# Optimization experiments

Measured on AMD Instinct MI355X. Metric: run time of the kernel, lower is better.

The kernel has to match this reference:

```python
import jax, jax.numpy as jnp
import numpy as np

B, MAX_OBJS, D = 8, 12, 512
NUM_OBJ, NUM_ACT, NUM_TRS = 37, 6, 3
EMBED = 128
NUM_AA = 100
NUM_CLASSES = 300
ACT_THRES = 0.5
K = MAX_OBJS * NUM_ACT            # 72 candidate (object, action) slots
FINAL_DIM = 2 * (D + 2 * EMBED)   # 1536
# All ordered pairs (i, j), i != j, in lexicographic order. itertools.permutations
# over a sorted index subset is exactly the valid-masked subsequence of this list.
_pairs = np.array([(i, j) for i in range(K) for j in range(K) if i != j], dtype=np.int64)
PAIR_I = jnp.asarray(_pairs[:, 0])
PAIR_J = jnp.asarray(_pairs[:, 1])
P = _pairs.shape[0]               # K*(K-1) = 5112 (static max num pairs)


def setup_inputs() -> dict:
    key = jax.random.key(0)
    ks = jax.random.split(key, 12)
    inp = jax.random.normal(ks[0], (B, MAX_OBJS, D), jnp.float32)
    objmask = jnp.ones((B, MAX_OBJS), jnp.float32)
    # -1 marks 'no composite-action target' for that (obj, act) slot
    AAidxs_tgts = jax.random.randint(ks[1], (B, K), -1, NUM_AA)
    TR_tgts = jax.random.uniform(ks[2], (B, K, K, NUM_TRS), jnp.float32)
    obj_act_lookup = jax.random.randint(ks[3], (NUM_OBJ, NUM_ACT), 0, NUM_AA)
    aa_aa_tr_lookup = jax.random.randint(ks[4], (NUM_AA, NUM_AA, NUM_TRS), 0, NUM_CLASSES)
    s = lambda k, shape: (jax.random.normal(k, shape, jnp.float32) * 0.02)
    return {
        'inp': inp, 'objmask': objmask,
        'TR_tgts': TR_tgts,
        'W_obj': s(ks[5], (NUM_OBJ, D)), 'b_obj': jnp.zeros((NUM_OBJ,), jnp.float32),
        'W_act': s(ks[6], (NUM_ACT, D)), 'b_act': jnp.zeros((NUM_ACT,), jnp.float32),
        'W_tr': s(ks[7], (NUM_TRS, FINAL_DIM)), 'b_tr': jnp.zeros((NUM_TRS,), jnp.float32),
        'W_ne': s(ks[8], (NUM_CLASSES, D)), 'b_ne': jnp.zeros((NUM_CLASSES,), jnp.float32),
        'obj_emb': s(ks[9], (NUM_OBJ, EMBED)), 'act_emb': s(ks[10], (NUM_ACT, EMBED)),
        'AAidxs_tgts': AAidxs_tgts,
        'obj_act_lookup': obj_act_lookup,
        'aa_aa_tr_lookup': aa_aa_tr_lookup,
    }


def reference(inp, objmask, TR_tgts, W_obj, b_obj, W_act, b_act, W_tr, b_tr,
              W_ne, b_ne, obj_emb, act_emb, AAidxs_tgts, obj_act_lookup,
              aa_aa_tr_lookup):
    # training branch (is_eval=False); obj_act_lookup only used in eval branch
    exp_objmask = jnp.repeat(objmask, NUM_ACT, axis=1)                # [B,K]
    masked = inp * objmask[:, :, None]
    pooled = masked.sum(axis=1) / objmask.sum(axis=1, keepdims=True)  # [B,D]
    non_exist_out = pooled @ W_ne.T + b_ne                            # [B,C]
    obj_out = inp @ W_obj.T + b_obj                                   # [B,MO,NO]
    act_out = inp @ W_act.T + b_act                                   # [B,MO,NA]

    posb_action_idxs = jnp.tile(jnp.arange(NUM_ACT), (B, MAX_OBJS))   # [B,K]
    pred_obj_idxs = jnp.repeat(jnp.argmax(obj_out, axis=-1), NUM_ACT, axis=1)  # [B,K]
    posb_inputs = jnp.repeat(inp, NUM_ACT, axis=1)                    # [B,K,D]

    pred_act = (jax.nn.sigmoid(act_out.reshape(B, K)) > ACT_THRES).astype(jnp.float32)
    pred_act = pred_act * exp_objmask
    selected = (pred_act == 1.0) & (AAidxs_tgts != -1)                # [B,K]
    aaidx = jnp.where(selected, AAidxs_tgts, -1)

    posb_obj_emb = obj_emb[pred_obj_idxs]                             # [B,K,E]
    posb_act_emb = act_emb[posb_action_idxs]                          # [B,K,E]
    comp = jnp.concatenate([posb_inputs, posb_obj_emb, posb_act_emb], axis=-1)  # [B,K,FINAL/2]

    # pack valid pairs to the front (stable sort preserves lexicographic order,
    # matching itertools.permutations over the sorted selected index set)
    valid = selected[:, PAIR_I] & selected[:, PAIR_J]                 # [B,P]
    order = jnp.argsort(~valid, axis=1, stable=True)                  # [B,P]
    valid_p = jnp.take_along_axis(valid, order, axis=1)
    i_p = jnp.take_along_axis(jnp.broadcast_to(PAIR_I, (B, P)), order, axis=1)
    j_p = jnp.take_along_axis(jnp.broadcast_to(PAIR_J, (B, P)), order, axis=1)
    b_ix = jnp.arange(B)[:, None]

    pair_out = jnp.where(valid_p[..., None],
                         jnp.concatenate([comp[b_ix, i_p], comp[b_ix, j_p]], axis=-1),
                         -1.0)                                        # [B,P,FINAL_DIM]
    pair_logits = pair_out @ W_tr.T + b_tr                            # [B,P,3]

    aai = aaidx[b_ix, i_p]
    aaj = aaidx[b_ix, j_p]
    ca = aa_aa_tr_lookup[jnp.maximum(aai, 0), jnp.maximum(aaj, 0)]    # [B,P,3]
    ca = jnp.where(valid_p[..., None], ca, -1)
    tr_targets = jnp.where(valid_p[..., None], TR_tgts[b_ix, i_p, j_p], -1.0)

    # diag(logit) @ one_hot(ca) then masked max over pairs == segment max per class
    flat_logit = pair_logits.reshape(B, P * NUM_TRS)
    flat_ca = ca.reshape(B, P * NUM_TRS)
    flat_valid = jnp.repeat(valid_p, NUM_TRS, axis=1)
    seg = jnp.where(flat_valid, flat_ca, NUM_CLASSES)                 # dump invalid to extra segment
    seg_max = jax.vmap(lambda l, s: jax.ops.segment_max(l, s, num_segments=NUM_CLASSES + 1))(
        flat_logit, seg)[:, :NUM_CLASSES]                             # [B,C]
    counts = jax.vmap(lambda s: jax.ops.segment_sum(jnp.ones_like(s), s, num_segments=NUM_CLASSES + 1))(
        seg)[:, :NUM_CLASSES]
    exist = counts > 0
    final_outputs = jnp.where(exist, seg_max, non_exist_out)          # [B,C]

    return final_outputs, pair_logits, tr_targets, act_out, obj_out
```

## Files before the change

kernel.cpp:

```cpp
#include <hip/hip_runtime.h>
#include <hip/hip_bf16.h>

#define Bn    8
#define MO    12
#define Dd    512
#define NOBJ  37
#define NACT  6
#define NTRS  3
#define EMB   128
#define NAA   100
#define NCLS  300
#define Kk    72
#define Pp    5112
#define HALF  768
#define FD    1536

#define OUT_FINAL 0
#define OUT_PLOG  (Bn*NCLS)
#define OUT_TTGT  (OUT_PLOG + Bn*Pp*NTRS)
#define OUT_ACT   (OUT_TTGT + Bn*Pp*NTRS)
#define OUT_OBJ   (OUT_ACT + Bn*Kk)

#define WS_POOL 0
#define WS_OBJ  (WS_POOL + Bn*Dd)
#define WS_ACT  (WS_OBJ + Bn*MO*NOBJ)
#define WS_LINP (WS_ACT + Bn*Kk)
#define WS_EO   (WS_LINP + Bn*MO*6)
#define WS_EA   (WS_EO + NOBJ*6)
#define WS_INV  (WS_EA + NACT*6)
#define WS_NE   (WS_INV + 6)
#define WS_SEG  (WS_NE + Bn*NCLS)
#define WS_PRED (WS_SEG + Bn*NCLS)
#define WS_SEL  (WS_PRED + Bn*MO)
#define WS_AAI  (WS_SEL + Bn*Kk)

__device__ __forceinline__ unsigned fmap(float f) {
  unsigned u = __float_as_uint(f);
  return (u & 0x80000000u) ? ~u : (u | 0x80000000u);
}
__device__ __forceinline__ float funmap(unsigned u) {
  return __uint_as_float((u & 0x80000000u) ? (u & 0x7fffffffu) : ~u);
}

__device__ __forceinline__ float wreduce(float v) {
#pragma unroll
  for (int off = 32; off > 0; off >>= 1) v += __shfl_xor(v, off, 64);
  return v;
}

__device__ __forceinline__ float dot512_wave(const float* __restrict__ a,
                                             const float* __restrict__ b, int lane) {
  const float4* a4 = (const float4*)a;
  const float4* b4 = (const float4*)b;
  float4 x0 = a4[lane], y0 = b4[lane];
  float4 x1 = a4[lane + 64], y1 = b4[lane + 64];
  float s0 = fmaf(x0.x, y0.x, fmaf(x0.y, y0.y, fmaf(x0.z, y0.z, x0.w * y0.w)));
  float s1 = fmaf(x1.x, y1.x, fmaf(x1.y, y1.y, fmaf(x1.z, y1.z, x1.w * y1.w)));
  return wreduce(s0 + s1);
}

__device__ __forceinline__ float dot128_wave(const float* __restrict__ a,
                                             const float* __restrict__ b, int lane) {
  const float2* a2 = (const float2*)a;
  const float2* b2 = (const float2*)b;
  float2 x = a2[lane], y = b2[lane];
  return wreduce(fmaf(x.x, y.x, x.y * y.y));
}

#define AW_OBJ  (Bn*MO*NOBJ)
#define AW_ACT  (AW_OBJ + Bn*Kk)
#define AW_LINP (AW_ACT + Bn*MO*6)
#define AW_EO   (AW_LINP + NOBJ*6)
#define AW_EA   (AW_EO + NACT*6)
#define AW_INV  (AW_EA + NTRS)
#define AW_POOL (AW_INV + Bn*8)
#define AW_ZERO (AW_POOL + 38)

__global__ __launch_bounds__(256) void kA(
    const float* __restrict__ inp, const float* __restrict__ objmask,
    const float* __restrict__ W_obj, const float* __restrict__ b_obj,
    const float* __restrict__ W_act, const float* __restrict__ b_act,
    const float* __restrict__ W_tr, const float* __restrict__ b_tr,
    const float* __restrict__ obj_emb, const float* __restrict__ act_emb,
    float* __restrict__ out, float* __restrict__ ws)
{
  int gt = blockIdx.x * 256 + threadIdx.x;
  int w = gt >> 6, lane = gt & 63;
  if (w < AW_OBJ) {
    int b = w / (MO*NOBJ), r = w % (MO*NOBJ), o = r / NOBJ, c = r % NOBJ;
    float v = dot512_wave(W_obj + c*Dd, inp + (b*MO+o)*Dd, lane) + b_obj[c];
    if (!lane) { out[OUT_OBJ + (b*MO+o)*NOBJ + c] = v; ws[WS_OBJ + (b*MO+o)*NOBJ + c] = v; }
  } else if (w < AW_ACT) {
    int r = w - AW_OBJ, b = r / Kk, k = r % Kk, o = k / NACT, a = k % NACT;
    float v = dot512_wave(W_act + a*Dd, inp + (b*MO+o)*Dd, lane) + b_act[a];
    if (!lane) { out[OUT_ACT + b*Kk + k] = v; ws[WS_ACT + b*Kk + k] = v; }
  } else if (w < AW_LINP) {
    int r = w - AW_ACT, b = r / (MO*6), r2 = r % (MO*6), o = r2 / 6, th = r2 % 6;
    int t = th >> 1, h = th & 1;
    float v = dot512_wave(W_tr + t*FD + h*HALF, inp + (b*MO+o)*Dd, lane);
    if (!lane) ws[WS_LINP + (b*MO+o)*6 + th] = v;
  } else if (w < AW_EO) {
    int r = w - AW_LINP, oc = r / 6, th = r % 6, t = th >> 1, h = th & 1;
    float v = dot128_wave(W_tr + t*FD + h*HALF + Dd, obj_emb + oc*EMB, lane);
    if (!lane) ws[WS_EO + oc*6 + th] = v;
  } else if (w < AW_EA) {
    int r = w - AW_EO, a = r / 6, th = r % 6, t = th >> 1, h = th & 1;
    float v = dot128_wave(W_tr + t*FD + h*HALF + Dd + EMB, act_emb + a*EMB, lane);
    if (!lane) ws[WS_EA + a*6 + th] = v;
  } else if (w < AW_INV) {
    int t = w - AW_EA;
    const float4* w4 = (const float4*)(W_tr + t*FD);
    float s = 0.f;
#pragma unroll
    for (int i = 0; i < 6; ++i) { float4 x = w4[lane + 64*i]; s += x.x + x.y + x.z + x.w; }
    s = wreduce(s);
    if (!lane) ws[WS_INV + t] = b_tr[t] - s;
  } else if (w < AW_POOL) {
    int r = w - AW_INV, b = r >> 3, d = (r & 7)*64 + lane;
    float msum = 0.f, acc = 0.f;
#pragma unroll
    for (int o = 0; o < MO; ++o) {
      float m = objmask[b*MO + o];
      msum += m;
      acc = fmaf(inp[(b*MO+o)*Dd + d], m, acc);
    }
    ws[WS_POOL + b*Dd + d] = acc / msum;
  } else if (w < AW_ZERO) {
    int idx = (w - AW_POOL)*64 + lane;
    if (idx < Bn*NCLS) ((unsigned*)ws)[WS_SEG + idx] = 0u;
  }
}

#define BW_NE (Bn*NCLS)

__global__ __launch_bounds__(256) void kB(
    const float* __restrict__ objmask, const int* __restrict__ AA,
    const float* __restrict__ W_ne, const float* __restrict__ b_ne,
    float* __restrict__ ws)
{
  int gt = blockIdx.x * 256 + threadIdx.x;
  int w = gt >> 6, lane = gt & 63;
  if (w < BW_NE) {
    int b = w / NCLS, c = w % NCLS;
    float v = dot512_wave(W_ne + c*Dd, ws + WS_POOL + b*Dd, lane) + b_ne[c];
    if (!lane) ws[WS_NE + b*NCLS + c] = v;
  } else {
    int t2 = gt - BW_NE*64;
    if (t2 < Bn*MO) {
      int b = t2 / MO, o = t2 % MO;
      const float* p = ws + WS_OBJ + (b*MO+o)*NOBJ;
      float best = p[0]; int bi = 0;
      for (int c = 1; c < NOBJ; ++c) { float v = p[c]; if (v > best) { best = v; bi = c; } }
      ((int*)ws)[WS_PRED + b*MO + o] = bi;
    } else if (t2 < Bn*MO + Bn*Kk) {
      int r = t2 - Bn*MO, b = r / Kk, k = r % Kk, o = k / NACT;
      int aa = AA[b*Kk + k];
      int sel = (ws[WS_ACT + b*Kk + k] > 0.f) && (objmask[b*MO+o] == 1.0f) && (aa != -1);
      ((int*)ws)[WS_SEL + b*Kk + k] = sel;
      ((int*)ws)[WS_AAI + b*Kk + k] = sel ? aa : -1;
    }
  }
}

#define NSLICE 20

__global__ __launch_bounds__(256) void kC(
    const float* __restrict__ TRt, const float* __restrict__ b_tr,
    const int* __restrict__ aalut,
    float* __restrict__ out, float* __restrict__ ws)
{
  __shared__ float s_L[Kk*6];
  __shared__ float s_inv[NTRS];
  __shared__ int s_sel[Kk], s_aa[Kk], s_C[Kk], s_T;

  int b = blockIdx.x / NSLICE, slice = blockIdx.x % NSLICE;
  int tid = threadIdx.x;

  if (tid < Kk) {
    s_sel[tid] = ((const int*)ws)[WS_SEL + b*Kk + tid];
    s_aa[tid]  = ((const int*)ws)[WS_AAI + b*Kk + tid];
  } else if (tid < Kk + NTRS) {
    s_inv[tid - Kk] = ws[WS_INV + (tid - Kk)];
  }
  for (int m = tid; m < Kk*6; m += 256) {
    int k = m / 6, th = m % 6, t = th >> 1, h = th & 1;
    int o = k / NACT, a = k % NACT;
    int po = ((const int*)ws)[WS_PRED + b*MO + o];
    float v = ws[WS_LINP + (b*MO+o)*6 + th] + ws[WS_EO + po*6 + th] + ws[WS_EA + a*6 + th];
    if (h == 0) v += b_tr[t];
    s_L[m] = v;
  }
  __syncthreads();
  if (tid == 0) {
    int c = 0;
    for (int k = 0; k < Kk; ++k) { s_C[k] = c; c += s_sel[k]; }
    s_T = c;
  }
  __syncthreads();

  int T = s_T, Vtot = T*(T-1);
  int q = slice*256 + tid;
  if (q < Pp) {
    float* plog = out + OUT_PLOG + (size_t)b*Pp*NTRS;
    float* ttgt = out + OUT_TTGT + (size_t)b*Pp*NTRS;
    int i = q / (Kk-1);
    int jj = q - i*(Kk-1);
    int j = jj + (jj >= i ? 1 : 0);
    int si = s_sel[i], sj = s_sel[j];
    int vb = s_C[i]*(T-1) + (si ? (s_C[j] - (i < j ? 1 : 0)) : 0);
    bool valid = si && sj;
    int pos = valid ? vb : (Vtot + q - vb);
    float l0, l1, l2;
    if (valid) {
      l0 = s_L[i*6+0] + s_L[j*6+1];
      l1 = s_L[i*6+2] + s_L[j*6+3];
      l2 = s_L[i*6+4] + s_L[j*6+5];
    } else { l0 = s_inv[0]; l1 = s_inv[1]; l2 = s_inv[2]; }
    int ob = pos*3;
    plog[ob+0] = l0; plog[ob+1] = l1; plog[ob+2] = l2;
    if (valid) {
      const float* tr = TRt + (((size_t)b*Kk + i)*Kk + j)*NTRS;
      ttgt[ob+0] = tr[0]; ttgt[ob+1] = tr[1]; ttgt[ob+2] = tr[2];
      int base = (s_aa[i]*NAA + s_aa[j])*NTRS;
      unsigned* seg = (unsigned*)ws + WS_SEG + b*NCLS;
      atomicMax(&seg[aalut[base+0]], fmap(l0));
      atomicMax(&seg[aalut[base+1]], fmap(l1));
      atomicMax(&seg[aalut[base+2]], fmap(l2));
    } else {
      ttgt[ob+0] = -1.f; ttgt[ob+1] = -1.f; ttgt[ob+2] = -1.f;
    }
  }
}

__global__ __launch_bounds__(320) void kD(float* __restrict__ out,
                                          const float* __restrict__ ws)
{
  int b = blockIdx.x, c = threadIdx.x;
  if (c < NCLS) {
    unsigned u = ((const unsigned*)ws)[WS_SEG + b*NCLS + c];
    out[OUT_FINAL + b*NCLS + c] = u ? funmap(u) : ws[WS_NE + b*NCLS + c];
  }
}

extern "C" void kernel_launch(void* const* d_in, const int* in_sizes, int n_in,
                              void* d_out, int out_size, void* d_ws, size_t ws_size,
                              hipStream_t stream) {
  (void)in_sizes; (void)n_in; (void)ws_size; (void)out_size;
  const float* inp      = (const float*)d_in[0];
  const float* objmask  = (const float*)d_in[1];
  const float* TRt      = (const float*)d_in[2];
  const float* W_obj    = (const float*)d_in[3];
  const float* b_obj    = (const float*)d_in[4];
  const float* W_act    = (const float*)d_in[5];
  const float* b_act    = (const float*)d_in[6];
  const float* W_tr     = (const float*)d_in[7];
  const float* b_tr     = (const float*)d_in[8];
  const float* W_ne     = (const float*)d_in[9];
  const float* b_ne     = (const float*)d_in[10];
  const float* obj_emb  = (const float*)d_in[11];
  const float* act_emb  = (const float*)d_in[12];
  const int*   AA       = (const int*)d_in[13];
  const int*   aalut    = (const int*)d_in[15];
  float* out = (float*)d_out;
  float* ws  = (float*)d_ws;

  hipLaunchKernelGGL(kA, dim3((AW_ZERO + 3) / 4), dim3(256), 0, stream,
                     inp, objmask, W_obj, b_obj, W_act, b_act, W_tr, b_tr,
                     obj_emb, act_emb, out, ws);
  hipLaunchKernelGGL(kB, dim3((BW_NE + 11 + 3) / 4), dim3(256), 0, stream,
                     objmask, AA, W_ne, b_ne, ws);
  hipLaunchKernelGGL(kC, dim3(Bn * NSLICE), dim3(256), 0, stream,
                     TRt, b_tr, aalut, out, ws);
  hipLaunchKernelGGL(kD, dim3(Bn), dim3(320), 0, stream, out, ws);
}
```

Before: 97.00 us.

## Fuse pooling, classifier heads and selection into one kernel, dropping a launch

Merges the first two kernels into one. Each object row is loaded once per wave and reused across all object-class and action dot products, and argmax and selection are computed in-wave. The masked mean pooling is recomputed inside every non-exist class wave, so no pooled intermediate goes through workspace. This removes one kernel launch and a global round trip. In exchange there is redundant pooling work (300 times per batch) and longer serial per-wave loops for the object head.

```diff
diff --git a/kernel.cpp b/kernel.cpp
--- a/kernel.cpp
+++ b/kernel.cpp
@@ -21,10 +21,7 @@
 #define OUT_ACT   (OUT_TTGT + Bn*Pp*NTRS)
 #define OUT_OBJ   (OUT_ACT + Bn*Kk)
 
-#define WS_POOL 0
-#define WS_OBJ  (WS_POOL + Bn*Dd)
-#define WS_ACT  (WS_OBJ + Bn*MO*NOBJ)
-#define WS_LINP (WS_ACT + Bn*Kk)
+#define WS_LINP 0
 #define WS_EO   (WS_LINP + Bn*MO*6)
 #define WS_EA   (WS_EO + NOBJ*6)
 #define WS_INV  (WS_EA + NACT*6)
@@ -48,15 +45,19 @@
   return v;
 }
 
+__device__ __forceinline__ float dotW(const float* __restrict__ wrow,
+                                      float4 x0, float4 x1, int lane) {
+  const float4* w4 = (const float4*)wrow;
+  float4 w0 = w4[lane], w1 = w4[lane + 64];
+  float s0 = fmaf(w0.x, x0.x, fmaf(w0.y, x0.y, fmaf(w0.z, x0.z, w0.w * x0.w)));
+  float s1 = fmaf(w1.x, x1.x, fmaf(w1.y, x1.y, fmaf(w1.z, x1.z, w1.w * x1.w)));
+  return wreduce(s0 + s1);
+}
+
 __device__ __forceinline__ float dot512_wave(const float* __restrict__ a,
                                              const float* __restrict__ b, int lane) {
-  const float4* a4 = (const float4*)a;
   const float4* b4 = (const float4*)b;
-  float4 x0 = a4[lane], y0 = b4[lane];
-  float4 x1 = a4[lane + 64], y1 = b4[lane + 64];
-  float s0 = fmaf(x0.x, y0.x, fmaf(x0.y, y0.y, fmaf(x0.z, y0.z, x0.w * y0.w)));
-  float s1 = fmaf(x1.x, y1.x, fmaf(x1.y, y1.y, fmaf(x1.z, y1.z, x1.w * y1.w)));
-  return wreduce(s0 + s1);
+  return dotW(a, b4[lane], b4[lane + 64], lane);
 }
 
 __device__ __forceinline__ float dot128_wave(const float* __restrict__ a,
@@ -67,104 +68,106 @@
   return wreduce(fmaf(x.x, y.x, x.y * y.y));
 }
 
-#define AW_OBJ  (Bn*MO*NOBJ)
-#define AW_ACT  (AW_OBJ + Bn*Kk)
-#define AW_LINP (AW_ACT + Bn*MO*6)
-#define AW_EO   (AW_LINP + NOBJ*6)
-#define AW_EA   (AW_EO + NACT*6)
-#define AW_INV  (AW_EA + NTRS)
-#define AW_POOL (AW_INV + Bn*8)
-#define AW_ZERO (AW_POOL + 38)
-
-__global__ __launch_bounds__(256) void kA(
+#define W_TOBJ  (Bn*MO)
+#define W_TACT  (W_TOBJ + Bn*MO)
+#define W_TLINP (W_TACT + Bn*MO*6)
+#define W_TEO   (W_TLINP + NOBJ*6)
+#define W_TEA   (W_TEO + NACT*6)
+#define W_TINV  (W_TEA + NTRS)
+#define W_TNE   (W_TINV + Bn*NCLS)
+#define W_TOT   (W_TNE + 38)
+
+__global__ __launch_bounds__(256) void k1(
     const float* __restrict__ inp, const float* __restrict__ objmask,
     const float* __restrict__ W_obj, const float* __restrict__ b_obj,
     const float* __restrict__ W_act, const float* __restrict__ b_act,
     const float* __restrict__ W_tr, const float* __restrict__ b_tr,
+    const float* __restrict__ W_ne, const float* __restrict__ b_ne,
     const float* __restrict__ obj_emb, const float* __restrict__ act_emb,
+    const int* __restrict__ AA,
     float* __restrict__ out, float* __restrict__ ws)
 {
   int gt = blockIdx.x * 256 + threadIdx.x;
   int w = gt >> 6, lane = gt & 63;
-  if (w < AW_OBJ) {
-    int b = w / (MO*NOBJ), r = w % (MO*NOBJ), o = r / NOBJ, c = r % NOBJ;
-    float v = dot512_wave(W_obj + c*Dd, inp + (b*MO+o)*Dd, lane) + b_obj[c];
-    if (!lane) { out[OUT_OBJ + (b*MO+o)*NOBJ + c] = v; ws[WS_OBJ + (b*MO+o)*NOBJ + c] = v; }
-  } else if (w < AW_ACT) {
-    int r = w - AW_OBJ, b = r / Kk, k = r % Kk, o = k / NACT, a = k % NACT;
-    float v = dot512_wave(W_act + a*Dd, inp + (b*MO+o)*Dd, lane) + b_act[a];
-    if (!lane) { out[OUT_ACT + b*Kk + k] = v; ws[WS_ACT + b*Kk + k] = v; }
-  } else if (w < AW_LINP) {
-    int r = w - AW_ACT, b = r / (MO*6), r2 = r % (MO*6), o = r2 / 6, th = r2 % 6;
+
+  if (w < W_TOBJ) {
+    int b = w / MO, o = w % MO;
+    const float4* x4 = (const float4*)(inp + (b*MO + o)*Dd);
+    float4 x0 = x4[lane], x1 = x4[lane + 64];
+    float myval = 0.f, best = 0.f;
+    int bi = 0;
+    for (int c = 0; c < NOBJ; ++c) {
+      float s = dotW(W_obj + c*Dd, x0, x1, lane) + b_obj[c];
+      if (lane == c) myval = s;
+      if (c == 0 || s > best) { best = s; bi = c; }
+    }
+    if (lane < NOBJ) out[OUT_OBJ + (b*MO + o)*NOBJ + lane] = myval;
+    if (lane == 0) ((int*)ws)[WS_PRED + b*MO + o] = bi;
+  } else if (w < W_TACT) {
+    int r = w - W_TOBJ, b = r / MO, o = r % MO;
+    const float4* x4 = (const float4*)(inp + (b*MO + o)*Dd);
+    float4 x0 = x4[lane], x1 = x4[lane + 64];
+    float myv = 0.f;
+    for (int a = 0; a < NACT; ++a) {
+      float s = dotW(W_act + a*Dd, x0, x1, lane) + b_act[a];
+      if (lane == a) myv = s;
+    }
+    if (lane < NACT) {
+      int k = o*NACT + lane;
+      out[OUT_ACT + b*Kk + k] = myv;
+      int aa = AA[b*Kk + k];
+      int sel = (myv > 0.f) && (objmask[b*MO + o] == 1.0f) && (aa != -1);
+      ((int*)ws)[WS_SEL + b*Kk + k] = sel;
+      ((int*)ws)[WS_AAI + b*Kk + k] = sel ? aa : -1;
+    }
+  } else if (w < W_TLINP) {
+    int r = w - W_TACT, b = r / (MO*6), r2 = r % (MO*6), o = r2 / 6, th = r2 % 6;
     int t = th >> 1, h = th & 1;
-    float v = dot512_wave(W_tr + t*FD + h*HALF, inp + (b*MO+o)*Dd, lane);
-    if (!lane) ws[WS_LINP + (b*MO+o)*6 + th] = v;
-  } else if (w < AW_EO) {
-    int r = w - AW_LINP, oc = r / 6, th = r % 6, t = th >> 1, h = th & 1;
+    float v = dot512_wave(W_tr + t*FD + h*HALF, inp + (b*MO + o)*Dd, lane);
+    if (!lane) ws[WS_LINP + (b*MO + o)*6 + th] = v;
+  } else if (w < W_TEO) {
+    int r = w - W_TLINP, oc = r / 6, th = r % 6, t = th >> 1, h = th & 1;
     float v = dot128_wave(W_tr + t*FD + h*HALF + Dd, obj_emb + oc*EMB, lane);
     if (!lane) ws[WS_EO + oc*6 + th] = v;
-  } else if (w < AW_EA) {
-    int r = w - AW_EO, a = r / 6, th = r % 6, t = th >> 1, h = th & 1;
+  } else if (w < W_TEA) {
+    int r = w - W_TEO, a = r / 6, th = r % 6, t = th >> 1, h = th & 1;
     float v = dot128_wave(W_tr + t*FD + h*HALF + Dd + EMB, act_emb + a*EMB, lane);
     if (!lane) ws[WS_EA + a*6 + th] = v;
-  } else if (w < AW_INV) {
-    int t = w - AW_EA;
+  } else if (w < W_TINV) {
+    int t = w - W_TEA;
     const float4* w4 = (const float4*)(W_tr + t*FD);
     float s = 0.f;
 #pragma unroll
     for (int i = 0; i < 6; ++i) { float4 x = w4[lane + 64*i]; s += x.x + x.y + x.z + x.w; }
     s = wreduce(s);
     if (!lane) ws[WS_INV + t] = b_tr[t] - s;
-  } else if (w < AW_POOL) {
-    int r = w - AW_INV, b = r >> 3, d = (r & 7)*64 + lane;
-    float msum = 0.f, acc = 0.f;
+  } else if (w < W_TNE) {
+    int r = w - W_TINV, b = r / NCLS, c = r % NCLS;
+    const float4* i4 = (const float4*)inp;
+    float msum = 0.f;
+    float4 p0 = make_float4(0.f, 0.f, 0.f, 0.f), p1 = p0;
 #pragma unroll
     for (int o = 0; o < MO; ++o) {
       float m = objmask[b*MO + o];
       msum += m;
-      acc = fmaf(inp[(b*MO+o)*Dd + d], m, acc);
-    }
-    ws[WS_POOL + b*Dd + d] = acc / msum;
-  } else if (w < AW_ZERO) {
-    int idx = (w - AW_POOL)*64 + lane;
+      float4 v0 = i4[(b*MO + o)*128 + lane];
+      float4 v1 = i4[(b*MO + o)*128 + lane + 64];
+      p0.x = fmaf(m, v0.x, p0.x); p0.y = fmaf(m, v0.y, p0.y);
+      p0.z = fmaf(m, v0.z, p0.z); p0.w = fmaf(m, v0.w, p0.w);
+      p1.x = fmaf(m, v1.x, p1.x); p1.y = fmaf(m, v1.y, p1.y);
+      p1.z = fmaf(m, v1.z, p1.z); p1.w = fmaf(m, v1.w, p1.w);
+    }
+    float v = dotW(W_ne + c*Dd, p0, p1, lane) / msum + b_ne[c];
+    if (!lane) ws[WS_NE + b*NCLS + c] = v;
+  } else if (w < W_TOT) {
+    int idx = (w - W_TNE)*64 + lane;
     if (idx < Bn*NCLS) ((unsigned*)ws)[WS_SEG + idx] = 0u;
   }
 }
 
-#define BW_NE (Bn*NCLS)
-
-__global__ __launch_bounds__(256) void kB(
-    const float* __restrict__ objmask, const int* __restrict__ AA,
-    const float* __restrict__ W_ne, const float* __restrict__ b_ne,
-    float* __restrict__ ws)
-{
-  int gt = blockIdx.x * 256 + threadIdx.x;
-  int w = gt >> 6, lane = gt & 63;
-  if (w < BW_NE) {
-    int b = w / NCLS, c = w % NCLS;
-    float v = dot512_wave(W_ne + c*Dd, ws + WS_POOL + b*Dd, lane) + b_ne[c];
-    if (!lane) ws[WS_NE + b*NCLS + c] = v;
-  } else {
-    int t2 = gt - BW_NE*64;
-    if (t2 < Bn*MO) {
-      int b = t2 / MO, o = t2 % MO;
-      const float* p = ws + WS_OBJ + (b*MO+o)*NOBJ;
-      float best = p[0]; int bi = 0;
-      for (int c = 1; c < NOBJ; ++c) { float v = p[c]; if (v > best) { best = v; bi = c; } }
-      ((int*)ws)[WS_PRED + b*MO + o] = bi;
-    } else if (t2 < Bn*MO + Bn*Kk) {
-      int r = t2 - Bn*MO, b = r / Kk, k = r % Kk, o = k / NACT;
-      int aa = AA[b*Kk + k];
-      int sel = (ws[WS_ACT + b*Kk + k] > 0.f) && (objmask[b*MO+o] == 1.0f) && (aa != -1);
-      ((int*)ws)[WS_SEL + b*Kk + k] = sel;
-      ((int*)ws)[WS_AAI + b*Kk + k] = sel ? aa : -1;
-    }
-  }
-}
-
 #define NSLICE 20
 
-__global__ __launch_bounds__(256) void kC(
+__global__ __launch_bounds__(256) void k2(
     const float* __restrict__ TRt, const float* __restrict__ b_tr,
     const int* __restrict__ aalut,
     float* __restrict__ out, float* __restrict__ ws)
@@ -186,7 +189,7 @@
     int k = m / 6, th = m % 6, t = th >> 1, h = th & 1;
     int o = k / NACT, a = k % NACT;
     int po = ((const int*)ws)[WS_PRED + b*MO + o];
-    float v = ws[WS_LINP + (b*MO+o)*6 + th] + ws[WS_EO + po*6 + th] + ws[WS_EA + a*6 + th];
+    float v = ws[WS_LINP + (b*MO + o)*6 + th] + ws[WS_EO + po*6 + th] + ws[WS_EA + a*6 + th];
     if (h == 0) v += b_tr[t];
     s_L[m] = v;
   }
@@ -232,7 +235,7 @@
   }
 }
 
-__global__ __launch_bounds__(320) void kD(float* __restrict__ out,
+__global__ __launch_bounds__(320) void k3(float* __restrict__ out,
                                           const float* __restrict__ ws)
 {
   int b = blockIdx.x, c = threadIdx.x;
@@ -264,12 +267,10 @@
   float* out = (float*)d_out;
   float* ws  = (float*)d_ws;
 
-  hipLaunchKernelGGL(kA, dim3((AW_ZERO + 3) / 4), dim3(256), 0, stream,
+  hipLaunchKernelGGL(k1, dim3((W_TOT + 3) / 4), dim3(256), 0, stream,
                      inp, objmask, W_obj, b_obj, W_act, b_act, W_tr, b_tr,
-                     obj_emb, act_emb, out, ws);
-  hipLaunchKernelGGL(kB, dim3((BW_NE + 11 + 3) / 4), dim3(256), 0, stream,
-                     objmask, AA, W_ne, b_ne, ws);
-  hipLaunchKernelGGL(kC, dim3(Bn * NSLICE), dim3(256), 0, stream,
+                     W_ne, b_ne, obj_emb, act_emb, AA, out, ws);
+  hipLaunchKernelGGL(k2, dim3(Bn * NSLICE), dim3(256), 0, stream,
                      TRt, b_tr, aalut, out, ws);
-  hipLaunchKernelGGL(kD, dim3(Bn), dim3(320), 0, stream, out, ws);
-}
+  hipLaunchKernelGGL(k3, dim3(Bn), dim3(320), 0, stream, out, ws);
+}
```

Result: slower. 102.2 us (+5.4%).
